# Kernel tuning notes

Measured on AMD Instinct MI355X. Metric: run time of the kernel, lower is better.

Reference implementation:

```python
import jax, jax.numpy as jnp
import numpy as np

L, N, HID, H = 3, 65536, 256, 8
D = HID // H
FF = 4 * HID
EPS = 1e-5


def setup_inputs() -> dict:
    key = jax.random.key(0)
    ks = jax.random.split(key, 10)
    def lin_w(k, fan_in, shape):
        bound = 1.0 / np.sqrt(fan_in)
        return jax.random.uniform(k, shape, jnp.float32, -bound, bound)
    return {
        "x":    jax.random.normal(ks[0], (N, HID), jnp.float32),
        "Wq":   lin_w(ks[1], HID, (L, HID, HID)),
        "bq":   lin_w(ks[2], HID, (L, HID)),
        "Wk":   lin_w(ks[3], HID, (L, HID, HID)),
        "bk":   lin_w(ks[4], HID, (L, HID)),
        "Wv":   lin_w(ks[5], HID, (L, HID, HID)),
        "bv":   lin_w(ks[6], HID, (L, HID)),
        "Wh":   lin_w(ks[7], HID, (L, HID, HID)),
        "bh":   lin_w(ks[7], HID, (L, HID)),
        "g1kv": jnp.ones((L, HID), jnp.float32),
        "b1kv": jnp.zeros((L, HID), jnp.float32),
        "g1q":  jnp.ones((L, HID), jnp.float32),
        "b1q":  jnp.zeros((L, HID), jnp.float32),
        "Wf1":  lin_w(ks[8], HID, (L, HID, FF)),
        "bf1":  lin_w(ks[8], HID, (L, FF)),
        "Wf2":  lin_w(ks[9], FF, (L, FF, HID)),
        "bf2":  lin_w(ks[9], FF, (L, HID)),
        "g2":   jnp.ones((L, HID), jnp.float32),
        "b2":   jnp.zeros((L, HID), jnp.float32),
    }


def _layernorm(t, g, b):
    m = t.mean(-1, keepdims=True)
    v = jnp.square(t - m).mean(-1, keepdims=True)
    return (t - m) * jax.lax.rsqrt(v + EPS) * g + b


def reference(x, Wq, bq, Wk, bk, Wv, bv, Wh, bh, g1kv, b1kv, g1q, b1q,
              Wf1, bf1, Wf2, bf2, g2, b2):
    def step(h, p):
        (wq, bq_, wk, bk_, wv, bv_, wh, bh_, g1k, b1k_, g1q_, b1q_,
         wf1, bf1_, wf2, bf2_, g2_, b2_) = p
        ln_kv = _layernorm(h, g1k, b1k_)
        ln_q = _layernorm(h, g1q_, b1q_)
        q = (ln_q @ wq + bq_).reshape(N, H, D)
        k = (ln_kv @ wk + bk_).reshape(N, H, D)
        v = (ln_kv @ wv + bv_).reshape(N, H, D)
        # torch.norm(., p=2) is the GLOBAL Frobenius norm (a scalar)
        q = q / jnp.linalg.norm(q)
        k = k / jnp.linalg.norm(k)
        # torch.einsum('nhd,hdd->nhd') takes the DIAGONAL of kvs[h,d,k];
        # diag_kv[h,d] = sum_n k[n,h,d]*v[n,h,d]
        diag_kv = jnp.einsum('nhd,nhd->hd', k, v)
        attn_num = q * diag_kv + v * N                       # [N,H,D]
        ks_sum = k.sum(axis=0)                               # [H,D]
        denom = jnp.einsum('nhd,hd->nh', q, ks_sum)[:, :, None] + N
        attn = (attn_num / denom).reshape(N, HID)
        h_pre = h + (attn @ wh + bh_)                        # dropout=0 (eval)
        ffn = jax.nn.gelu(_layernorm(h_pre, g2_, b2_) @ wf1 + bf1_,
                          approximate=False) @ wf2 + bf2_
        return h_pre + ffn, None

    out, _ = jax.lax.scan(step, x, (Wq, bq, Wk, bk, Wv, bv, Wh, bh,
                                    g1kv, b1kv, g1q, b1q,
                                    Wf1, bf1, Wf2, bf2, g2, b2))
    return out
```

## Files before the change

kernel.cpp:

```cpp
#include <hip/hip_runtime.h>
#include <math.h>

#define N_TOK 65536
#define HID   256
#define FFDIM 1024
#define QKVM  768
#define EPS_LN 1e-5f

typedef __bf16 bf16x8 __attribute__((ext_vector_type(8)));
typedef __bf16 bf16x4 __attribute__((ext_vector_type(4)));
typedef float  f32x4  __attribute__((ext_vector_type(4)));
typedef unsigned short u16x8 __attribute__((ext_vector_type(8)));

__device__ __forceinline__ float gelu_f(float x) {
    const float t = 1.59576912f * x * fmaf(0.044715f, x * x, 1.0f);
    return x / (1.0f + __expf(-t));
}
__device__ __forceinline__ float bf2f(unsigned short u) {
    return __uint_as_float(((unsigned int)u) << 16);
}
__device__ __forceinline__ unsigned short f2bf(float f) {
    unsigned int x = __float_as_uint(f);
    unsigned int r = ((x >> 16) & 1u) + 0x7fffu;
    return (unsigned short)((x + r) >> 16);
}

__global__ __launch_bounds__(256) void wconv(
    const float* __restrict__ src, const float* __restrict__ g,
    unsigned short* __restrict__ dst,
    const int K, const int M, const size_t dstLS, const int moff, const int mstride)
{
    const int l = blockIdx.z;
    __shared__ float t[32][33];
    const int r  = threadIdx.x >> 3;
    const int c0 = (threadIdx.x & 7) * 4;
    const int bk = blockIdx.x * 32;
    const int bm = blockIdx.y * 32;
    float4 v4 = *(const float4*)(src + (size_t)l * K * M + (size_t)(bk + r) * M + bm + c0);
    if (g) {
        const float gv = g[(size_t)l * K + bk + r];
        v4.x *= gv; v4.y *= gv; v4.z *= gv; v4.w *= gv;
    }
    t[r][c0] = v4.x; t[r][c0+1] = v4.y; t[r][c0+2] = v4.z; t[r][c0+3] = v4.w;
    __syncthreads();
    ushort4 o;
    o.x = f2bf(t[c0+0][r]);
    o.y = f2bf(t[c0+1][r]);
    o.z = f2bf(t[c0+2][r]);
    o.w = f2bf(t[c0+3][r]);
    *(ushort4*)(dst + (size_t)l * dstLS +
                (size_t)(moff + (bm + r) * mstride) * K + bk + c0) = o;
}

__global__ __launch_bounds__(256) void biasfold(
    const float* __restrict__ W, const float* __restrict__ bias,
    const float* __restrict__ bvec, float* __restrict__ outb,
    const int K, const int M, const size_t outLS, const int moff, const int mstride)
{
    const int l = blockIdx.y;
    const int m = blockIdx.x * 256 + threadIdx.x;
    float acc = bias[(size_t)l * M + m];
    const float* Wl = W + (size_t)l * K * M;
    const float* bv = bvec + (size_t)l * K;
    for (int k = 0; k < K; ++k) acc = fmaf(bv[k], Wl[(size_t)k * M + m], acc);
    outb[(size_t)l * outLS + moff + m * mstride] = acc;
}

__global__ __launch_bounds__(256) void colsum(
    const unsigned short* __restrict__ wt, float* __restrict__ S, const int M)
{
    const int l = blockIdx.y;
    const int j = blockIdx.x * 256 + threadIdx.x;
    const unsigned short* rowp = wt + (size_t)l * M * HID + (size_t)j * HID;
    float s = 0.f;
    for (int k = 0; k < HID; k += 8) {
        const u16x8 u = *(const u16x8*)(rowp + k);
        #pragma unroll
        for (int t = 0; t < 8; ++t) s += bf2f(u[t]);
    }
    S[(size_t)l * M + j] = s;
}

__global__ __launch_bounds__(256) void cast_stats(
    const float* __restrict__ x, unsigned short* __restrict__ hb,
    float* __restrict__ mean, float* __restrict__ rstd)
{
    const int row  = blockIdx.x * 4 + (threadIdx.x >> 6);
    const int lane = threadIdx.x & 63;
    const size_t base = (size_t)row * HID + lane * 4;
    const float4 xv = *(const float4*)(x + base);
    ushort4 o;
    o.x = f2bf(xv.x); o.y = f2bf(xv.y); o.z = f2bf(xv.z); o.w = f2bf(xv.w);
    *(ushort4*)(hb + base) = o;
    float s  = xv.x + xv.y + xv.z + xv.w;
    float s2 = fmaf(xv.x, xv.x, fmaf(xv.y, xv.y, fmaf(xv.z, xv.z, xv.w * xv.w)));
    #pragma unroll
    for (int off = 32; off > 0; off >>= 1) {
        s  += __shfl_xor(s, off, 64);
        s2 += __shfl_xor(s2, off, 64);
    }
    if (lane == 0) {
        const float m   = s * (1.0f / HID);
        const float var = fmaxf(s2 * (1.0f / HID) - m * m, 0.f);
        mean[row] = m;
        rstd[row] = rsqrtf(var + EPS_LN);
    }
}

template<int K, bool LNEP, bool GELU_EP, bool REDUCE, bool OUTF32>
__global__ __launch_bounds__(256, 2) void gemm_rs(
    const unsigned short* __restrict__ A, const int lda,
    const unsigned short* __restrict__ Wt,
    const float* __restrict__ Bias, const float* __restrict__ S,
    const float* __restrict__ mean, const float* __restrict__ rstd,
    void* __restrict__ C, const int ldc, const int nCT,
    unsigned short* __restrict__ Cv,
    float* __restrict__ pkv, float* __restrict__ pks,
    float* __restrict__ psq, float* __restrict__ psk)
{
    constexpr int KT  = K / 32;
    constexpr int LDT = 40;
    __shared__ __align__(16) unsigned short Abuf[2][256 * LDT];
    __shared__ __align__(16) unsigned short Bbuf[2][128 * LDT];
    __shared__ float redKV[2][64];
    __shared__ float redKS[2][64];
    __shared__ float sredS[4];
    const int tid = threadIdx.x;
    const int gsz = nCT << 3;
    const int grp = blockIdx.x / gsz;
    const int rem = blockIdx.x - grp * gsz;
    const int bm  = ((grp << 3) + (rem & 7)) << 8;
    const int bn  = (rem >> 3) << 7;
    const int lr = tid >> 2;
    const int lk = (tid & 3) << 3;
    const unsigned short* Ag = A  + (size_t)(bm + lr) * lda + lk;
    const unsigned short* Bg = Wt + (size_t)(bn + lr) * K   + lk;
    const int lds_off = lr * LDT + lk;

    const int lane = tid & 63;
    const int wv   = tid >> 6;
    const int wr   = (wv >> 1) << 7;
    const int wc   = (wv & 1) << 6;
    const int lrow = lane & 15;
    const int kgrp = lane >> 4;

    f32x4 acc[8][4];
    #pragma unroll
    for (int i = 0; i < 8; ++i)
        #pragma unroll
        for (int j = 0; j < 4; ++j)
            acc[i][j] = (f32x4){0.f, 0.f, 0.f, 0.f};

    u16x8 aA0, aA1, aA2, aA3, bA0, bA1;
    u16x8 aB0, aB1, aB2, aB3, bB0, bB1;
    #define GLOADA_RS(kt) { const unsigned short* a_ = Ag + (kt) * 32;           \
        const unsigned short* b_ = Bg + (kt) * 32;                               \
        aA0 = *(const u16x8*)a_;                                                 \
        aA1 = *(const u16x8*)(a_ + (size_t)64  * lda);                           \
        aA2 = *(const u16x8*)(a_ + (size_t)128 * lda);                           \
        aA3 = *(const u16x8*)(a_ + (size_t)192 * lda);                           \
        bA0 = *(const u16x8*)b_;                                                 \
        bA1 = *(const u16x8*)(b_ + (size_t)64 * K); }
    #define GLOADB_RS(kt) { const unsigned short* a_ = Ag + (kt) * 32;           \
        const unsigned short* b_ = Bg + (kt) * 32;                               \
        aB0 = *(const u16x8*)a_;                                                 \
        aB1 = *(const u16x8*)(a_ + (size_t)64  * lda);                           \
        aB2 = *(const u16x8*)(a_ + (size_t)128 * lda);                           \
        aB3 = *(const u16x8*)(a_ + (size_t)192 * lda);                           \
        bB0 = *(const u16x8*)b_;                                                 \
        bB1 = *(const u16x8*)(b_ + (size_t)64 * K); }
    #define LSTOREA_RS(buf) {                                                    \
        *(u16x8*)&Abuf[buf][lds_off]             = aA0;                          \
        *(u16x8*)&Abuf[buf][lds_off + 64  * LDT] = aA1;                          \
        *(u16x8*)&Abuf[buf][lds_off + 128 * LDT] = aA2;                          \
        *(u16x8*)&Abuf[buf][lds_off + 192 * LDT] = aA3;                          \
        *(u16x8*)&Bbuf[buf][lds_off]             = bA0;                          \
        *(u16x8*)&Bbuf[buf][lds_off + 64  * LDT] = bA1; }
    #define LSTOREB_RS(buf) {                                                    \
        *(u16x8*)&Abuf[buf][lds_off]             = aB0;                          \
        *(u16x8*)&Abuf[buf][lds_off + 64  * LDT] = aB1;                          \
        *(u16x8*)&Abuf[buf][lds_off + 128 * LDT] = aB2;                          \
        *(u16x8*)&Abuf[buf][lds_off + 192 * LDT] = aB3;                          \
        *(u16x8*)&Bbuf[buf][lds_off]             = bB0;                          \
        *(u16x8*)&Bbuf[buf][lds_off + 64  * LDT] = bB1; }
    #define MFMAS_RS(buf) {                                                      \
        bf16x8 af[8], bfr[4];                                                    \
        _Pragma("unroll")                                                        \
        for (int ni = 0; ni < 4; ++ni)                                           \
            bfr[ni] = *(const bf16x8*)&Bbuf[buf][(wc + ni * 16 + lrow) * LDT + kgrp * 8]; \
        _Pragma("unroll")                                                        \
        for (int mi = 0; mi < 8; ++mi)                                           \
            af[mi] = *(const bf16x8*)&Abuf[buf][(wr + mi * 16 + lrow) * LDT + kgrp * 8]; \
        _Pragma("unroll")                                                        \
        for (int mi = 0; mi < 8; ++mi)                                           \
            _Pragma("unroll")                                                    \
            for (int ni = 0; ni < 4; ++ni)                                       \
                acc[mi][ni] = __builtin_amdgcn_mfma_f32_16x16x32_bf16(           \
                    bfr[ni], af[mi], acc[mi][ni], 0, 0, 0); }

    GLOADA_RS(0);
    GLOADB_RS(1);
    LSTOREA_RS(0);
    __syncthreads();
    #pragma unroll
    for (int kt2 = 0; kt2 < KT; kt2 += 2) {
        LSTOREB_RS(1);
        if (kt2 + 2 < KT) GLOADA_RS(kt2 + 2);
        MFMAS_RS(0);
        __syncthreads();
        if (kt2 + 2 < KT) {
            LSTOREA_RS(0);
            if (kt2 + 3 < KT) GLOADB_RS(kt2 + 3);
        }
        MFMAS_RS(1);
        if (kt2 + 2 < KT) __syncthreads();
    }
    #undef GLOADA_RS
    #undef GLOADB_RS
    #undef LSTOREA_RS
    #undef LSTOREB_RS
    #undef MFMAS_RS

    float4 bcol[4], scol[4];
    #pragma unroll
    for (int ni = 0; ni < 4; ++ni) {
        const int col0 = bn + wc + ni * 16 + (kgrp << 2);
        bcol[ni] = *(const float4*)(Bias + col0);
        if (LNEP) scol[ni] = *(const float4*)(S + col0);
    }
    const bool isQ = (bn < 256);
    float acKV[4][2] = {}, acKS[4][2] = {};
    float scal1 = 0.f;
    #pragma unroll
    for (int mi = 0; mi < 8; ++mi) {
        const int row = bm + wr + mi * 16 + lrow;
        float mrow = 0.f, rsrow = 0.f;
        if (LNEP) { mrow = mean[row]; rsrow = rstd[row]; }
        const size_t rowC = (size_t)row * ldc;
        #pragma unroll
        for (int ni = 0; ni < 4; ++ni) {
            const int col0 = bn + wc + ni * 16 + (kgrp << 2);
            float v[4];
            #pragma unroll
            for (int r = 0; r < 4; ++r) v[r] = acc[mi][ni][r];
            if (LNEP) {
                v[0] = fmaf(v[0] - mrow * scol[ni].x, rsrow, bcol[ni].x);
                v[1] = fmaf(v[1] - mrow * scol[ni].y, rsrow, bcol[ni].y);
                v[2] = fmaf(v[2] - mrow * scol[ni].z, rsrow, bcol[ni].z);
                v[3] = fmaf(v[3] - mrow * scol[ni].w, rsrow, bcol[ni].w);
            } else {
                v[0] += bcol[ni].x; v[1] += bcol[ni].y;
                v[2] += bcol[ni].z; v[3] += bcol[ni].w;
            }
            if (GELU_EP) {
                v[0] = gelu_f(v[0]); v[1] = gelu_f(v[1]);
                v[2] = gelu_f(v[2]); v[3] = gelu_f(v[3]);
            }
            if (REDUCE && !isQ) {
                acKV[ni][0] = fmaf(v[0], v[1], acKV[ni][0]);
                acKV[ni][1] = fmaf(v[2], v[3], acKV[ni][1]);
                acKS[ni][0] += v[0];
                acKS[ni][1] += v[2];
                scal1 = fmaf(v[0], v[0], fmaf(v[2], v[2], scal1));
                const unsigned int pk2 =
                    (unsigned int)f2bf(v[1]) | ((unsigned int)f2bf(v[3]) << 16);
                *(unsigned int*)(Cv + (size_t)row * HID + ((col0 - 256) >> 1)) = pk2;
            } else {
                if (REDUCE) {
                    scal1 = fmaf(v[0], v[0], fmaf(v[1], v[1],
                             fmaf(v[2], v[2], fmaf(v[3], v[3], scal1))));
                }
                if (OUTF32) {
                    float4 o = {v[0], v[1], v[2], v[3]};
                    *(float4*)((float*)C + rowC + col0) = o;
                } else {
                    bf16x4 o = {(__bf16)v[0], (__bf16)v[1], (__bf16)v[2], (__bf16)v[3]};
                    *(bf16x4*)((unsigned short*)C + rowC + col0) = o;
                }
            }
        }
    }
    if (REDUCE) {
        const int rowG = bm >> 8;
        #pragma unroll
        for (int off = 32; off > 0; off >>= 1) scal1 += __shfl_xor(scal1, off, 64);
        if (lane == 0) sredS[wv] = scal1;
        if (!isQ) {
            #pragma unroll
            for (int ni = 0; ni < 4; ++ni)
                #pragma unroll
                for (int pr = 0; pr < 2; ++pr) {
                    float a = acKV[ni][pr], b = acKS[ni][pr];
                    #pragma unroll
                    for (int off = 1; off < 16; off <<= 1) {
                        a += __shfl_xor(a, off, 64);
                        b += __shfl_xor(b, off, 64);
                    }
                    if (lrow == 0) {
                        const int p = (wc >> 1) + ni * 8 + (kgrp << 1) + pr;
                        redKV[wv >> 1][p] = a;
                        redKS[wv >> 1][p] = b;
                    }
                }
        }
        __syncthreads();
        if (tid == 0) {
            const float t = sredS[0] + sredS[1] + sredS[2] + sredS[3];
            if (isQ) psq[rowG * 2 + (bn >> 7)] = t;
            else     psk[rowG * 4 + ((bn - 256) >> 7)] = t;
        }
        if (!isQ && tid < 64) {
            const int cb = (bn - 256) >> 1;
            pkv[(size_t)rowG * 256 + cb + tid] = redKV[0][tid] + redKV[1][tid];
            pks[(size_t)rowG * 256 + cb + tid] = redKS[0][tid] + redKS[1][tid];
        }
    }
}

template<int K, bool ATTN, bool STATS, bool OUTF32>
__global__ __launch_bounds__(256, 2) void gemm_rn(
    const unsigned short* __restrict__ A, const int lda,
    const unsigned short* __restrict__ Av,
    const unsigned short* __restrict__ Wt,
    const float* __restrict__ Bias,
    const unsigned short* __restrict__ res,
    void* __restrict__ C,
    float* __restrict__ meanO, float* __restrict__ rstdO,
    const float* __restrict__ kvs, const float* __restrict__ kss,
    const float* __restrict__ scal)
{
    constexpr int KT  = K / 32;
    constexpr int LDT = 40;
    __shared__ __align__(16) unsigned short Abuf[2][128 * LDT];
    __shared__ __align__(16) unsigned short Bbuf[2][256 * LDT];
    __shared__ float sredS[128][2];
    __shared__ float sredQ[128][2];
    const int tid = threadIdx.x;
    const int bm  = blockIdx.x << 7;
    const int lr = tid >> 2;
    const int lk = (tid & 3) << 3;
    const unsigned short* Ag = A  + (size_t)(bm + lr) * lda + lk;
    const unsigned short* Bg = Wt + (size_t)lr * K + lk;
    const int lds_off = lr * LDT + lk;

    const int lane = tid & 63;
    const int wv   = tid >> 6;
    const int wr   = (wv >> 1) << 6;
    const int wc   = (wv & 1) << 7;
    const int lrow = lane & 15;
    const int kgrp = lane >> 4;

    const float inv = ATTN ? scal[0] : 0.f;

    f32x4 acc[4][8];
    #pragma unroll
    for (int i = 0; i < 4; ++i)
        #pragma unroll
        for (int j = 0; j < 8; ++j)
            acc[i][j] = (f32x4){0.f, 0.f, 0.f, 0.f};

    u16x8 ra0, ra1, rb0, rb1, rb2, rb3;
    auto gload = [&](int kt) {
        const unsigned short* b = Bg + kt * 32;
        rb0 = *(const u16x8*)b;
        rb1 = *(const u16x8*)(b + (size_t)64  * K);
        rb2 = *(const u16x8*)(b + (size_t)128 * K);
        rb3 = *(const u16x8*)(b + (size_t)192 * K);
        if constexpr (ATTN) {
            const int col = kt * 32 + lk;
            float kvsL[8], kssL[8];
            *(float4*)&kvsL[0] = *(const float4*)(kvs + col);
            *(float4*)&kvsL[4] = *(const float4*)(kvs + col + 4);
            *(float4*)&kssL[0] = *(const float4*)(kss + col);
            *(float4*)&kssL[4] = *(const float4*)(kss + col + 4);
            #pragma unroll
            for (int half = 0; half < 2; ++half) {
                const size_t rbase = (size_t)(bm + lr + half * 64) * 256;
                const u16x8 q8 = *(const u16x8*)(A  + rbase + col);
                const u16x8 v8 = *(const u16x8*)(Av + rbase + col);
                float qf[8];
                float dot = 0.f;
                #pragma unroll
                for (int j = 0; j < 8; ++j) {
                    qf[j] = bf2f(q8[j]);
                    dot = fmaf(qf[j], kssL[j], dot);
                }
                dot += __shfl_xor(dot, 1, 4);
                dot += __shfl_xor(dot, 2, 4);
                const float rden = 1.0f / fmaf(dot, inv, (float)N_TOK);
                u16x8 o;
                #pragma unroll
                for (int j = 0; j < 8; ++j)
                    o[j] = f2bf(fmaf(qf[j] * kvsL[j], inv,
                                     bf2f(v8[j]) * (float)N_TOK) * rden);
                if (half == 0) ra0 = o; else ra1 = o;
            }
        } else {
            const unsigned short* a = Ag + kt * 32;
            ra0 = *(const u16x8*)a;
            ra1 = *(const u16x8*)(a + (size_t)64 * lda);
        }
    };
    auto lstore = [&](int buf) {
        *(u16x8*)&Abuf[buf][lds_off]             = ra0;
        *(u16x8*)&Abuf[buf][lds_off + 64 * LDT]  = ra1;
        *(u16x8*)&Bbuf[buf][lds_off]             = rb0;
        *(u16x8*)&Bbuf[buf][lds_off + 64  * LDT] = rb1;
        *(u16x8*)&Bbuf[buf][lds_off + 128 * LDT] = rb2;
        *(u16x8*)&Bbuf[buf][lds_off + 192 * LDT] = rb3;
    };

    gload(0);
    lstore(0);
    __syncthreads();
    for (int kt = 0; kt < KT; ++kt) {
        const int cur = kt & 1;
        if (kt + 1 < KT) gload(kt + 1);
        bf16x8 af[4], bfr[8];
        #pragma unroll
        for (int ni = 0; ni < 8; ++ni)
            bfr[ni] = *(const bf16x8*)&Bbuf[cur][(wc + ni * 16 + lrow) * LDT + kgrp * 8];
        #pragma unroll
        for (int mi = 0; mi < 4; ++mi)
            af[mi] = *(const bf16x8*)&Abuf[cur][(wr + mi * 16 + lrow) * LDT + kgrp * 8];
        #pragma unroll
        for (int mi = 0; mi < 4; ++mi)
            #pragma unroll
            for (int ni = 0; ni < 8; ++ni)
                acc[mi][ni] = __builtin_amdgcn_mfma_f32_16x16x32_bf16(
                    bfr[ni], af[mi], acc[mi][ni], 0, 0, 0);
        if (kt + 1 < KT) {
            lstore(cur ^ 1);
            __syncthreads();
        }
    }
    float sS[4], sQ[4];
    #pragma unroll
    for (int mi = 0; mi < 4; ++mi) { sS[mi] = 0.f; sQ[mi] = 0.f; }
    #pragma unroll
    for (int mi = 0; mi < 4; ++mi) {
        const int row = bm + wr + mi * 16 + lrow;
        const size_t rowC = (size_t)row * HID;
        #pragma unroll
        for (int ni = 0; ni < 8; ++ni) {
            const int col0 = wc + ni * 16 + (kgrp << 2);
            const float4 bcol = *(const float4*)(Bias + col0);
            const ushort4 rv = *(const ushort4*)(res + rowC + col0);
            float v[4];
            #pragma unroll
            for (int r = 0; r < 4; ++r) v[r] = acc[mi][ni][r];
            v[0] += bcol.x + bf2f(rv.x);
            v[1] += bcol.y + bf2f(rv.y);
            v[2] += bcol.z + bf2f(rv.z);
            v[3] += bcol.w + bf2f(rv.w);
            if (STATS) {
                sS[mi] += v[0] + v[1] + v[2] + v[3];
                sQ[mi] = fmaf(v[0], v[0], fmaf(v[1], v[1],
                          fmaf(v[2], v[2], fmaf(v[3], v[3], sQ[mi]))));
            }
            if (OUTF32) {
                float4 o = {v[0], v[1], v[2], v[3]};
                *(float4*)((float*)C + rowC + col0) = o;
            } else {
                bf16x4 o = {(__bf16)v[0], (__bf16)v[1], (__bf16)v[2], (__bf16)v[3]};
                *(bf16x4*)((unsigned short*)C + rowC + col0) = o;
            }
        }
    }
    if (STATS) {
        #pragma unroll
        for (int mi = 0; mi < 4; ++mi) {
            sS[mi] += __shfl_xor(sS[mi], 16, 64);
            sS[mi] += __shfl_xor(sS[mi], 32, 64);
            sQ[mi] += __shfl_xor(sQ[mi], 16, 64);
            sQ[mi] += __shfl_xor(sQ[mi], 32, 64);
        }
        __syncthreads();
        if (lane < 16) {
            #pragma unroll
            for (int mi = 0; mi < 4; ++mi) {
                const int ridx = wr + mi * 16 + lrow;
                sredS[ridx][wv & 1] = sS[mi];
                sredQ[ridx][wv & 1] = sQ[mi];
            }
        }
        __syncthreads();
        if ((wv & 1) == 0 && lane < 16) {
            #pragma unroll
            for (int mi = 0; mi < 4; ++mi) {
                const int ridx = wr + mi * 16 + lrow;
                const float Ssum = sredS[ridx][0] + sredS[ridx][1];
                const float Qsum = sredQ[ridx][0] + sredQ[ridx][1];
                const float m    = Ssum * (1.0f / HID);
                const float var  = fmaxf(Qsum * (1.0f / HID) - m * m, 0.f);
                meanO[bm + ridx] = m;
                rstdO[bm + ridx] = rsqrtf(var + EPS_LN);
            }
        }
    }
}

__global__ __launch_bounds__(256) void finalize_kernel(
    const float* __restrict__ pkv, const float* __restrict__ pks,
    const float* __restrict__ psq, const float* __restrict__ psk,
    float* __restrict__ kvsum, float* __restrict__ kssum, float* __restrict__ scal)
{
    const int blk = blockIdx.x;
    const int tid = threadIdx.x;
    if (blk < 32) {
        const int col = blk * 8 + (tid >> 5);
        const int sub = tid & 31;
        float kv = 0.f, ks = 0.f;
        #pragma unroll
        for (int j = 0; j < 8; ++j) {
            const int rg = sub + (j << 5);
            kv += pkv[(size_t)rg * HID + col];
            ks += pks[(size_t)rg * HID + col];
        }
        #pragma unroll
        for (int off = 16; off > 0; off >>= 1) {
            kv += __shfl_xor(kv, off, 32);
            ks += __shfl_xor(ks, off, 32);
        }
        if (sub == 0) { kvsum[col] = kv; kssum[col] = ks; }
    } else {
        float sq = psq[tid] + psq[tid + 256];
        float sk = psk[tid] + psk[tid + 256] + psk[tid + 512] + psk[tid + 768];
        #pragma unroll
        for (int off = 32; off > 0; off >>= 1) {
            sq += __shfl_xor(sq, off, 64);
            sk += __shfl_xor(sk, off, 64);
        }
        __shared__ float s1[4], s2[4];
        if ((tid & 63) == 0) { s1[tid >> 6] = sq; s2[tid >> 6] = sk; }
        __syncthreads();
        if (tid == 0) {
            const float SQ = s1[0] + s1[1] + s1[2] + s1[3];
            const float SK = s2[0] + s2[1] + s2[2] + s2[3];
            scal[0] = rsqrtf(SQ * SK);
        }
    }
}

extern "C" void kernel_launch(void* const* d_in, const int* in_sizes, int n_in,
                              void* d_out, int out_size, void* d_ws, size_t ws_size,
                              hipStream_t stream) {
    const float* x    = (const float*)d_in[0];
    const float* Wq   = (const float*)d_in[1];
    const float* bq   = (const float*)d_in[2];
    const float* Wk   = (const float*)d_in[3];
    const float* bk   = (const float*)d_in[4];
    const float* Wv   = (const float*)d_in[5];
    const float* bv   = (const float*)d_in[6];
    const float* Wh   = (const float*)d_in[7];
    const float* bh   = (const float*)d_in[8];
    const float* g1kv = (const float*)d_in[9];
    const float* b1kv = (const float*)d_in[10];
    const float* g1q  = (const float*)d_in[11];
    const float* b1q  = (const float*)d_in[12];
    const float* Wf1  = (const float*)d_in[13];
    const float* bf1  = (const float*)d_in[14];
    const float* Wf2  = (const float*)d_in[15];
    const float* bf2  = (const float*)d_in[16];
    const float* g2   = (const float*)d_in[17];
    const float* b2   = (const float*)d_in[18];
    float* out = (float*)d_out;

    char* p = (char*)d_ws;
    const size_t nh = (size_t)N_TOK * HID;
    unsigned short* hb   = (unsigned short*)p; p += nh * 2;
    unsigned short* hpre = (unsigned short*)p; p += nh * 2;
    unsigned short* act  = (unsigned short*)p;
    unsigned short* qbuf = act;
    unsigned short* vbuf = act + nh;
    p += nh * 8;
    float* meanb = (float*)p; p += N_TOK * sizeof(float);
    float* rstdb = (float*)p; p += N_TOK * sizeof(float);
    unsigned short* wtqkv = (unsigned short*)p; p += (size_t)3 * QKVM * HID * 2;
    unsigned short* wth   = (unsigned short*)p; p += (size_t)3 * HID * HID * 2;
    unsigned short* wtf1  = (unsigned short*)p; p += (size_t)3 * FFDIM * HID * 2;
    unsigned short* wtf2  = (unsigned short*)p; p += (size_t)3 * HID * FFDIM * 2;
    float* bqkv = (float*)p; p += (size_t)3 * QKVM * sizeof(float);
    float* bf1f = (float*)p; p += (size_t)3 * FFDIM * sizeof(float);
    float* Sqkv = (float*)p; p += (size_t)3 * QKVM * sizeof(float);
    float* Sf1  = (float*)p; p += (size_t)3 * FFDIM * sizeof(float);
    float* pkv  = (float*)p; p += (size_t)256 * HID * sizeof(float);
    float* pks  = (float*)p; p += (size_t)256 * HID * sizeof(float);
    float* psq  = (float*)p; p += 512 * sizeof(float);
    float* psk  = (float*)p; p += 1024 * sizeof(float);
    float* kvs  = (float*)p; p += HID * sizeof(float);
    float* kss  = (float*)p; p += HID * sizeof(float);
    float* scal = (float*)p; p += 256;

    const size_t qkvLS = (size_t)QKVM * HID;
    wconv<<<dim3(8, 8, 3),  256, 0, stream>>>(Wq,  g1q,  wtqkv, HID, HID, qkvLS, 0,   1);
    wconv<<<dim3(8, 8, 3),  256, 0, stream>>>(Wk,  g1kv, wtqkv, HID, HID, qkvLS, 256, 2);
    wconv<<<dim3(8, 8, 3),  256, 0, stream>>>(Wv,  g1kv, wtqkv, HID, HID, qkvLS, 257, 2);
    wconv<<<dim3(8, 8, 3),  256, 0, stream>>>(Wh,  nullptr, wth, HID, HID, (size_t)HID * HID, 0, 1);
    wconv<<<dim3(8, 32, 3), 256, 0, stream>>>(Wf1, g2,   wtf1, HID, FFDIM, (size_t)FFDIM * HID, 0, 1);
    wconv<<<dim3(32, 8, 3), 256, 0, stream>>>(Wf2, nullptr, wtf2, FFDIM, HID, (size_t)HID * FFDIM, 0, 1);
    colsum<<<dim3(3, 3), 256, 0, stream>>>(wtqkv, Sqkv, QKVM);
    colsum<<<dim3(4, 3), 256, 0, stream>>>(wtf1,  Sf1,  FFDIM);
    biasfold<<<dim3(1, 3), 256, 0, stream>>>(Wq,  bq,  b1q,  bqkv, HID, HID, QKVM, 0,   1);
    biasfold<<<dim3(1, 3), 256, 0, stream>>>(Wk,  bk,  b1kv, bqkv, HID, HID, QKVM, 256, 2);
    biasfold<<<dim3(1, 3), 256, 0, stream>>>(Wv,  bv,  b1kv, bqkv, HID, HID, QKVM, 257, 2);
    biasfold<<<dim3(4, 3), 256, 0, stream>>>(Wf1, bf1, b2,   bf1f, HID, FFDIM, FFDIM, 0, 1);
    cast_stats<<<N_TOK / 4, 256, 0, stream>>>(x, hb, meanb, rstdb);

    const int gQKV = (N_TOK / 256) * (QKVM / 128);
    const int gF1  = (N_TOK / 256) * (FFDIM / 128);
    const int gRN  = N_TOK / 128;

    for (int l = 0; l < 3; ++l) {
        gemm_rs<HID, true, false, true, false><<<gQKV, 256, 0, stream>>>(
            hb, HID, wtqkv + l * qkvLS, bqkv + l * QKVM, Sqkv + l * QKVM,
            meanb, rstdb, qbuf, HID, QKVM / 128, vbuf, pkv, pks, psq, psk);
        finalize_kernel<<<33, 256, 0, stream>>>(pkv, pks, psq, psk, kvs, kss, scal);
        gemm_rn<HID, true, true, false><<<gRN, 256, 0, stream>>>(
            qbuf, HID, vbuf, wth + (size_t)l * HID * HID, bh + (size_t)l * HID,
            hb, hpre, meanb, rstdb, kvs, kss, scal);
        gemm_rs<HID, true, true, false, false><<<gF1, 256, 0, stream>>>(
            hpre, HID, wtf1 + (size_t)l * FFDIM * HID, bf1f + (size_t)l * FFDIM,
            Sf1 + (size_t)l * FFDIM, meanb, rstdb, act, FFDIM, FFDIM / 128,
            nullptr, nullptr, nullptr, nullptr, nullptr);
        if (l < 2)
            gemm_rn<FFDIM, false, true, false><<<gRN, 256, 0, stream>>>(
                act, FFDIM, nullptr, wtf2 + (size_t)l * HID * FFDIM,
                bf2 + (size_t)l * HID, hpre, hb, meanb, rstdb,
                nullptr, nullptr, nullptr);
        else
            gemm_rn<FFDIM, false, false, true><<<gRN, 256, 0, stream>>>(
                act, FFDIM, nullptr, wtf2 + (size_t)l * HID * FFDIM,
                bf2 + (size_t)l * HID, hpre, out, meanb, rstdb,
                nullptr, nullptr, nullptr);
    }
}
```

Measured before the change: 924.2 us.

## Add 256x256-tile 512-thread GEMM with direct global-to-LDS loads for FFN

Introduces a new GEMM kernel with 256x256 output tiles, 8 waves per block and 64-wide K steps. Operands are staged with global_load_lds so data goes straight into LDS without passing through registers. It replaces the FFN1 and FFN2 GEMMs, and FFN2 now computes next-layer LayerNorm row statistics in its epilogue through a shared-memory reduction across waves. Larger tiles raise operand reuse, but occupancy drops to one block per CU. The LDS layout is unpadded, so the fragment reads may hit bank conflicts.

After: 968.6 us. +4.8%, slower.

```diff
diff --git a/kernel.cpp b/kernel.cpp
--- a/kernel.cpp
+++ b/kernel.cpp
@@ -23,6 +23,11 @@
     unsigned int x = __float_as_uint(f);
     unsigned int r = ((x >> 16) & 1u) + 0x7fffu;
     return (unsigned short)((x + r) >> 16);
+}
+__device__ __forceinline__ void gload16(const void* g, void* l) {
+    __builtin_amdgcn_global_load_lds(
+        (const __attribute__((address_space(1))) void*)g,
+        (__attribute__((address_space(3))) void*)l, 16, 0, 0);
 }
 
 __global__ __launch_bounds__(256) void wconv(
@@ -104,6 +109,160 @@
         const float var = fmaxf(s2 * (1.0f / HID) - m * m, 0.f);
         mean[row] = m;
         rstd[row] = rsqrtf(var + EPS_LN);
+    }
+}
+
+template<int K, bool LNEP, bool GELU_EP, bool RES, bool STATS, bool OUTF32>
+__global__ __launch_bounds__(512, 1) void gemm_2p(
+    const unsigned short* __restrict__ A, const int lda,
+    const unsigned short* __restrict__ Wt,
+    const float* __restrict__ Bias, const float* __restrict__ S,
+    const float* __restrict__ mean, const float* __restrict__ rstd,
+    const unsigned short* __restrict__ res,
+    void* __restrict__ C, const int ldc, const int nCT,
+    float* __restrict__ meanO, float* __restrict__ rstdO)
+{
+    constexpr int KT = K / 64;
+    __shared__ __align__(16) unsigned short Ab[2][256 * 64];
+    __shared__ __align__(16) unsigned short Bb[2][256 * 64];
+    __shared__ float sredS[256][4];
+    __shared__ float sredQ[256][4];
+    const int tid = threadIdx.x;
+    const int gsz = nCT << 3;
+    const int grp = blockIdx.x / gsz;
+    const int rem = blockIdx.x - grp * gsz;
+    const int bm  = ((grp << 3) + (rem & 7)) << 8;
+    const int bn  = (rem >> 3) << 8;
+    const unsigned short* As = A  + (size_t)(bm + (tid >> 3)) * lda + ((tid & 7) << 3);
+    const unsigned short* Bs = Wt + (size_t)(bn + (tid >> 3)) * K   + ((tid & 7) << 3);
+    const int lane = tid & 63;
+    const int wid  = tid >> 6;
+    const int wrow = (wid >> 2) << 7;
+    const int wcol = (wid & 3) << 6;
+    const int lrow = lane & 15;
+    const int kgrp = lane >> 4;
+
+    f32x4 acc[8][4];
+    #pragma unroll
+    for (int i = 0; i < 8; ++i)
+        #pragma unroll
+        for (int j = 0; j < 4; ++j)
+            acc[i][j] = (f32x4){0.f, 0.f, 0.f, 0.f};
+
+    auto STAGE = [&](int buf, int kt) {
+        const size_t ko = (size_t)kt * 64;
+        unsigned short* ad = &Ab[buf][wid << 9];
+        unsigned short* bd = &Bb[buf][wid << 9];
+        #pragma unroll
+        for (int i = 0; i < 4; ++i) {
+            gload16(As + (size_t)(i * 64) * lda + ko, ad + i * 4096);
+            gload16(Bs + (size_t)(i * 64) * K   + ko, bd + i * 4096);
+        }
+    };
+
+    STAGE(0, 0);
+    __syncthreads();
+    for (int kt = 0; kt < KT; ++kt) {
+        const int cur = kt & 1;
+        if (kt + 1 < KT) STAGE(cur ^ 1, kt + 1);
+        #pragma unroll
+        for (int ks = 0; ks < 2; ++ks) {
+            bf16x8 af[8], bfr[4];
+            #pragma unroll
+            for (int ni = 0; ni < 4; ++ni)
+                bfr[ni] = *(const bf16x8*)&Bb[cur][(wcol + ni * 16 + lrow) * 64 + ks * 32 + kgrp * 8];
+            #pragma unroll
+            for (int mi = 0; mi < 8; ++mi)
+                af[mi] = *(const bf16x8*)&Ab[cur][(wrow + mi * 16 + lrow) * 64 + ks * 32 + kgrp * 8];
+            #pragma unroll
+            for (int mi = 0; mi < 8; ++mi)
+                #pragma unroll
+                for (int ni = 0; ni < 4; ++ni)
+                    acc[mi][ni] = __builtin_amdgcn_mfma_f32_16x16x32_bf16(
+                        bfr[ni], af[mi], acc[mi][ni], 0, 0, 0);
+        }
+        __syncthreads();
+    }
+    float4 bcol[4], scol[4];
+    #pragma unroll
+    for (int ni = 0; ni < 4; ++ni) {
+        const int col0 = bn + wcol + ni * 16 + (kgrp << 2);
+        bcol[ni] = *(const float4*)(Bias + col0);
+        if (LNEP) scol[ni] = *(const float4*)(S + col0);
+    }
+    float sS[8], sQ[8];
+    #pragma unroll
+    for (int mi = 0; mi < 8; ++mi) { sS[mi] = 0.f; sQ[mi] = 0.f; }
+    #pragma unroll
+    for (int mi = 0; mi < 8; ++mi) {
+        const int row = bm + wrow + mi * 16 + lrow;
+        float mrow = 0.f, rsrow = 0.f;
+        if (LNEP) { mrow = mean[row]; rsrow = rstd[row]; }
+        const size_t rowC = (size_t)row * ldc;
+        const size_t rowR = RES ? (size_t)row * HID : 0;
+        #pragma unroll
+        for (int ni = 0; ni < 4; ++ni) {
+            const int col0 = bn + wcol + ni * 16 + (kgrp << 2);
+            float v[4];
+            #pragma unroll
+            for (int r = 0; r < 4; ++r) v[r] = acc[mi][ni][r];
+            if (LNEP) {
+                v[0] = fmaf(v[0] - mrow * scol[ni].x, rsrow, bcol[ni].x);
+                v[1] = fmaf(v[1] - mrow * scol[ni].y, rsrow, bcol[ni].y);
+                v[2] = fmaf(v[2] - mrow * scol[ni].z, rsrow, bcol[ni].z);
+                v[3] = fmaf(v[3] - mrow * scol[ni].w, rsrow, bcol[ni].w);
+            } else {
+                v[0] += bcol[ni].x; v[1] += bcol[ni].y;
+                v[2] += bcol[ni].z; v[3] += bcol[ni].w;
+            }
+            if (RES) {
+                const ushort4 rv = *(const ushort4*)(res + rowR + col0);
+                v[0] += bf2f(rv.x); v[1] += bf2f(rv.y);
+                v[2] += bf2f(rv.z); v[3] += bf2f(rv.w);
+            }
+            if (GELU_EP) {
+                v[0] = gelu_f(v[0]); v[1] = gelu_f(v[1]);
+                v[2] = gelu_f(v[2]); v[3] = gelu_f(v[3]);
+            }
+            if (STATS) {
+                sS[mi] += v[0] + v[1] + v[2] + v[3];
+                sQ[mi] = fmaf(v[0], v[0], fmaf(v[1], v[1],
+                          fmaf(v[2], v[2], fmaf(v[3], v[3], sQ[mi]))));
+            }
+            if (OUTF32) {
+                float4 o = {v[0], v[1], v[2], v[3]};
+                *(float4*)((float*)C + rowC + col0) = o;
+            } else {
+                bf16x4 o = {(__bf16)v[0], (__bf16)v[1], (__bf16)v[2], (__bf16)v[3]};
+                *(bf16x4*)((unsigned short*)C + rowC + col0) = o;
+            }
+        }
+    }
+    if (STATS) {
+        #pragma unroll
+        for (int mi = 0; mi < 8; ++mi) {
+            sS[mi] += __shfl_xor(sS[mi], 16, 64);
+            sS[mi] += __shfl_xor(sS[mi], 32, 64);
+            sQ[mi] += __shfl_xor(sQ[mi], 16, 64);
+            sQ[mi] += __shfl_xor(sQ[mi], 32, 64);
+        }
+        if (lane < 16) {
+            #pragma unroll
+            for (int mi = 0; mi < 8; ++mi) {
+                const int ridx = wrow + mi * 16 + lrow;
+                sredS[ridx][wid & 3] = sS[mi];
+                sredQ[ridx][wid & 3] = sQ[mi];
+            }
+        }
+        __syncthreads();
+        if (tid < 256) {
+            const float Ssum = sredS[tid][0] + sredS[tid][1] + sredS[tid][2] + sredS[tid][3];
+            const float Qsum = sredQ[tid][0] + sredQ[tid][1] + sredQ[tid][2] + sredQ[tid][3];
+            const float m    = Ssum * (1.0f / HID);
+            const float var  = fmaxf(Qsum * (1.0f / HID) - m * m, 0.f);
+            meanO[bm + tid] = m;
+            rstdO[bm + tid] = rsqrtf(var + EPS_LN);
+        }
     }
 }
 
@@ -608,8 +767,9 @@
     cast_stats<<<N_TOK / 4, 256, 0, stream>>>(x, hb, meanb, rstdb);
 
     const int gQKV = (N_TOK / 256) * (QKVM / 128);
-    const int gF1  = (N_TOK / 256) * (FFDIM / 128);
     const int gRN  = N_TOK / 128;
+    const int gF1  = (N_TOK / 256) * (FFDIM / 256);
+    const int gF2  = N_TOK / 256;
 
     for (int l = 0; l < 3; ++l) {
         gemm_rs<HID, true, false, true, false><<<gQKV, 256, 0, stream>>>(
@@ -619,19 +779,17 @@
         gemm_rn<HID, true, true, false><<<gRN, 256, 0, stream>>>(
             qbuf, HID, vbuf, wth + (size_t)l * HID * HID, bh + (size_t)l * HID,
             hb, hpre, meanb, rstdb, kvs, kss, scal);
-        gemm_rs<HID, true, true, false, false><<<gF1, 256, 0, stream>>>(
+        gemm_2p<HID, true, true, false, false, false><<<gF1, 512, 0, stream>>>(
             hpre, HID, wtf1 + (size_t)l * FFDIM * HID, bf1f + (size_t)l * FFDIM,
-            Sf1 + (size_t)l * FFDIM, meanb, rstdb, act, FFDIM, FFDIM / 128,
-            nullptr, nullptr, nullptr, nullptr, nullptr);
+            Sf1 + (size_t)l * FFDIM, meanb, rstdb, nullptr, act, FFDIM, 4,
+            nullptr, nullptr);
         if (l < 2)
-            gemm_rn<FFDIM, false, true, false><<<gRN, 256, 0, stream>>>(
-                act, FFDIM, nullptr, wtf2 + (size_t)l * HID * FFDIM,
-                bf2 + (size_t)l * HID, hpre, hb, meanb, rstdb,
-                nullptr, nullptr, nullptr);
+            gemm_2p<FFDIM, false, false, true, true, false><<<gF2, 512, 0, stream>>>(
+                act, FFDIM, wtf2 + (size_t)l * HID * FFDIM, bf2 + (size_t)l * HID,
+                nullptr, nullptr, nullptr, hpre, hb, HID, 1, meanb, rstdb);
         else
-            gemm_rn<FFDIM, false, false, true><<<gRN, 256, 0, stream>>>(
-                act, FFDIM, nullptr, wtf2 + (size_t)l * HID * FFDIM,
-                bf2 + (size_t)l * HID, hpre, out, meanb, rstdb,
-                nullptr, nullptr, nullptr);
-    }
-}
+            gemm_2p<FFDIM, false, false, true, false, true><<<gF2, 512, 0, stream>>>(
+                act, FFDIM, wtf2 + (size_t)l * HID * FFDIM, bf2 + (size_t)l * HID,
+                nullptr, nullptr, nullptr, hpre, out, HID, 1, nullptr, nullptr);
+    }
+}
```
